# Optimization experiments

Measured on AMD Instinct MI355X. Metric: run time of the kernel, lower is better.

Reference implementation:

```python
import jax, jax.numpy as jnp
import numpy as np

N = 50000      # num nodes
E0 = 400000    # raw directed edges
F = 64         # latent_dim (in and per-head out)
H = 2          # num_heads
L = 2          # num_layers
NEG_SLOPE = 0.2


def _build_edges(src_raw, dst_raw):
    # dgl.to_bidirected(dgl.graph((src,dst))) then add_self_loop
    s = np.asarray(src_raw, dtype=np.int64)
    d = np.asarray(dst_raw, dtype=np.int64)
    s2 = np.concatenate([s, d])
    d2 = np.concatenate([d, s])
    code = np.unique(s2 * N + d2)                      # dedupe (bidirected simple graph)
    s2, d2 = code // N, code % N
    keep = s2 != d2                                    # drop existing self loops
    s2, d2 = s2[keep], d2[keep]
    loops = np.arange(N, dtype=np.int64)
    s2 = np.concatenate([s2, loops])
    d2 = np.concatenate([d2, loops])
    return jnp.asarray(s2, jnp.int32), jnp.asarray(d2, jnp.int32)


def setup_inputs() -> dict:
    key = jax.random.key(0)
    kh, ks, kd, kw1, kb1, kw2, kb2, ka = jax.random.split(key, 8)
    src_raw = jax.random.randint(ks, (E0,), 0, N, dtype=jnp.int32)
    dst_raw = jax.random.randint(kd, (E0,), 0, N, dtype=jnp.int32)
    src, dst = _build_edges(np.asarray(src_raw), np.asarray(dst_raw))
    h = jax.random.normal(kh, (N, F), dtype=jnp.float32)
    scale = 1.0 / np.sqrt(F)
    Wsrc = jax.random.normal(kw1, (L, F, H * F), dtype=jnp.float32) * scale
    bsrc = jnp.zeros((L, H * F), dtype=jnp.float32)
    Wdst = jax.random.normal(kw2, (L, F, H * F), dtype=jnp.float32) * scale
    bdst = jnp.zeros((L, H * F), dtype=jnp.float32)
    attn = jax.random.normal(ka, (L, H, F), dtype=jnp.float32) * scale
    return {"h": h, "Wsrc": Wsrc, "bsrc": bsrc, "Wdst": Wdst, "bdst": bdst,
            "attn": attn, "src": src, "dst": dst}


def _gatv2_layer(h, Wsrc, bsrc, Wdst, bdst, attn, src, dst):
    # h: [N,F] -> per-head projections [N,H,F]
    fs = (h @ Wsrc + bsrc).reshape(N, H, F)
    fd = (h @ Wdst + bdst).reshape(N, H, F)
    # per-edge GATv2 logits: a^T leaky_relu(W_s h_u + W_d h_v)
    e = jax.nn.leaky_relu(fs[src] + fd[dst], NEG_SLOPE)      # [E,H,F]
    logits = jnp.einsum("ehf,hf->eh", e, attn)               # [E,H]
    # edge-softmax over incoming edges of each dst node
    m = jax.ops.segment_max(logits, dst, num_segments=N)     # [N,H]
    ex = jnp.exp(logits - m[dst])
    denom = jax.ops.segment_sum(ex, dst, num_segments=N)     # [N,H]
    alpha = ex / denom[dst]                                  # [E,H]
    # scatter-weighted aggregation
    out = jax.ops.segment_sum(alpha[:, :, None] * fs[src], dst, num_segments=N)  # [N,H,F]
    return out.mean(axis=1)                                  # head mean -> [N,F]


def reference(h, Wsrc, bsrc, Wdst, bdst, attn, src, dst):
    for l in range(L):
        h = _gatv2_layer(h, Wsrc[l], bsrc[l], Wdst[l], bdst[l], attn[l], src, dst)
    return h
```

## Files before the change

kernel.cpp:

```cpp
#include <hip/hip_runtime.h>


#define RLN2 1.4426950408889634f

typedef _Float16 half4v __attribute__((ext_vector_type(4)));

template <int CTRL>
__device__ __forceinline__ float dpp_add(float x) {
  return x + __int_as_float(__builtin_amdgcn_update_dpp(
                 0, __float_as_int(x), CTRL, 0xF, 0xF, true));
}

__device__ __forceinline__ float xor16_add(float x) {
  return x + __int_as_float(
                 __builtin_amdgcn_ds_swizzle(__float_as_int(x), 0x401F));
}

__global__ void rowstart_kernel(const int* __restrict__ src,
                                int* __restrict__ row_start, int EM, int n) {
  int v = blockIdx.x * blockDim.x + threadIdx.x;
  if (v > n) return;
  if (v == n) { row_start[n] = EM; return; }
  int lo = 0, hi = EM;
  while (lo < hi) {
    int mid = (lo + hi) >> 1;
    if (src[mid] < v) lo = mid + 1; else hi = mid;
  }
  row_start[v] = lo;
}

__global__ __launch_bounds__(512) void proj2_kernel(
    const float* __restrict__ hin, const float* __restrict__ Ws,
    const float* __restrict__ bs, const float* __restrict__ Wd,
    const float* __restrict__ bd, _Float16* __restrict__ fs16,
    float* __restrict__ fd, int n) {
  __shared__ float lds[12544];
  int tid = threadIdx.x;
  int tile = blockIdx.x >> 1;
  int half = blockIdx.x & 1;
  int fb = half * 32;
  int row0 = tile * 64;

  const float4* Ws4 = (const float4*)Ws;
  const float4* Wd4 = (const float4*)Wd;
#pragma unroll
  for (int t = 0; t < 2; ++t) {
    int g = tid + t * 512;
    int k = g >> 4, part = (g >> 3) & 1, c4 = g & 7;
    int srcf4 = k * 32 + part * 16 + half * 8 + c4;
    float4 vs = Ws4[srcf4];
    float4 vd = Wd4[srcf4];
    int base = k * 64 + 8 * c4 + part;
    lds[base + 0] = vs.x; lds[base + 2] = vs.y;
    lds[base + 4] = vs.z; lds[base + 6] = vs.w;
    lds[4096 + base + 0] = vd.x; lds[4096 + base + 2] = vd.y;
    lds[4096 + base + 4] = vd.z; lds[4096 + base + 6] = vd.w;
  }
  const float4* h4 = (const float4*)hin;
#pragma unroll
  for (int t = 0; t < 2; ++t) {
    int idx = tid + t * 512;
    int r = idx >> 4, c = idx & 15;
    int rr = min(row0 + r, n - 1);
    *(float4*)&lds[8192 + r * 68 + c * 4] = h4[(size_t)rr * 16 + c];
  }
  __syncthreads();

  const float* WsL = lds;
  const float* WdL = lds + 4096;
  const float* hL = lds + 8192;

  int jh = tid & 15;
  int rg = tid >> 4;
  int r0 = rg * 2;

  float4 as0 = make_float4(0, 0, 0, 0), as1 = make_float4(0, 0, 0, 0);
  float4 ad0 = make_float4(0, 0, 0, 0), ad1 = make_float4(0, 0, 0, 0);

#pragma unroll 4
  for (int k4 = 0; k4 < 16; ++k4) {
    float4 hv0 = *(const float4*)&hL[r0 * 68 + k4 * 4];
    float4 hv1 = *(const float4*)&hL[(r0 + 1) * 68 + k4 * 4];
    float h0a[4] = {hv0.x, hv0.y, hv0.z, hv0.w};
    float h1a[4] = {hv1.x, hv1.y, hv1.z, hv1.w};
#pragma unroll
    for (int kk = 0; kk < 4; ++kk) {
      int k = k4 * 4 + kk;
      float4 ws = *(const float4*)&WsL[k * 64 + jh * 4];
      float4 wd = *(const float4*)&WdL[k * 64 + jh * 4];
      as0.x = fmaf(h0a[kk], ws.x, as0.x); as0.y = fmaf(h0a[kk], ws.y, as0.y);
      as0.z = fmaf(h0a[kk], ws.z, as0.z); as0.w = fmaf(h0a[kk], ws.w, as0.w);
      as1.x = fmaf(h1a[kk], ws.x, as1.x); as1.y = fmaf(h1a[kk], ws.y, as1.y);
      as1.z = fmaf(h1a[kk], ws.z, as1.z); as1.w = fmaf(h1a[kk], ws.w, as1.w);
      ad0.x = fmaf(h0a[kk], wd.x, ad0.x); ad0.y = fmaf(h0a[kk], wd.y, ad0.y);
      ad0.z = fmaf(h0a[kk], wd.z, ad0.z); ad0.w = fmaf(h0a[kk], wd.w, ad0.w);
      ad1.x = fmaf(h1a[kk], wd.x, ad1.x); ad1.y = fmaf(h1a[kk], wd.y, ad1.y);
      ad1.z = fmaf(h1a[kk], wd.z, ad1.z); ad1.w = fmaf(h1a[kk], wd.w, ad1.w);
    }
  }

  int j0 = fb + 2 * jh, j1 = j0 + 1;
  float4 bsv = make_float4(bs[j0], bs[64 + j0], bs[j1], bs[64 + j1]);
  float4 bdv = make_float4(bd[j0], bd[64 + j0], bd[j1], bd[64 + j1]);
  int col = half * 16 + jh;
  float4* fd4 = (float4*)fd;
  half4v* fsH = (half4v*)fs16;
#pragma unroll
  for (int r = 0; r < 2; ++r) {
    int rr = row0 + r0 + r;
    if (rr < n) {
      float4 a = r ? as1 : as0;
      float4 d = r ? ad1 : ad0;
      fd4[(size_t)rr * 32 + col] = make_float4(d.x + bdv.x, d.y + bdv.y,
                                               d.z + bdv.z, d.w + bdv.w);
      half4v hv;
      hv.x = (_Float16)(a.x + bsv.x); hv.y = (_Float16)(a.y + bsv.y);
      hv.z = (_Float16)(a.z + bsv.z); hv.w = (_Float16)(a.w + bsv.w);
      fsH[(size_t)rr * 32 + col] = hv;
    }
  }
}

__global__ __launch_bounds__(256) void gat_node_kernel(
    const _Float16* __restrict__ fs16, const float* __restrict__ fd,
    const float* __restrict__ attn, const int* __restrict__ row_start,
    const int* __restrict__ nbr, float* __restrict__ out, int n) {
  int wid = (int)((blockIdx.x * 256 + threadIdx.x) >> 6);
  int lane = threadIdx.x & 63;
  if (wid >= n) return;
  int lp = lane & 15;
  int slot = lane >> 4;

  float aAx = attn[2 * lp] * RLN2;
  float aAy = attn[64 + 2 * lp] * RLN2;
  float aAz = attn[2 * lp + 1] * RLN2;
  float aAw = attn[64 + 2 * lp + 1] * RLN2;
  float aBx = attn[32 + 2 * lp] * RLN2;
  float aBy = attn[96 + 2 * lp] * RLN2;
  float aBz = attn[32 + 2 * lp + 1] * RLN2;
  float aBw = attn[96 + 2 * lp + 1] * RLN2;

  const half4v* fsH = (const half4v*)fs16;
  const float4* fd4 = (const float4*)fd;
  float4 fdA = fd4[(size_t)wid * 32 + lp];
  float4 fdB = fd4[(size_t)wid * 32 + 16 + lp];

  float4 accA = make_float4(0, 0, 0, 0), accB = make_float4(0, 0, 0, 0);
  float d0 = 0.f, d1 = 0.f;

  {
    half4v sa = fsH[(size_t)wid * 32 + lp];
    half4v sb = fsH[(size_t)wid * 32 + 16 + lp];
    float4 xA = make_float4((float)sa.x, (float)sa.y, (float)sa.z, (float)sa.w);
    float4 xB = make_float4((float)sb.x, (float)sb.y, (float)sb.z, (float)sb.w);
    float t, m, p0, p1;
    t = xA.x + fdA.x; m = fmaxf(t, 0.2f * t); p0 = aAx * m;
    t = xA.y + fdA.y; m = fmaxf(t, 0.2f * t); p1 = aAy * m;
    t = xA.z + fdA.z; m = fmaxf(t, 0.2f * t); p0 = fmaf(aAz, m, p0);
    t = xA.w + fdA.w; m = fmaxf(t, 0.2f * t); p1 = fmaf(aAw, m, p1);
    t = xB.x + fdB.x; m = fmaxf(t, 0.2f * t); p0 = fmaf(aBx, m, p0);
    t = xB.y + fdB.y; m = fmaxf(t, 0.2f * t); p1 = fmaf(aBy, m, p1);
    t = xB.z + fdB.z; m = fmaxf(t, 0.2f * t); p0 = fmaf(aBz, m, p0);
    t = xB.w + fdB.w; m = fmaxf(t, 0.2f * t); p1 = fmaf(aBw, m, p1);
    p0 = dpp_add<0xB1>(p0);  p1 = dpp_add<0xB1>(p1);
    p0 = dpp_add<0x4E>(p0);  p1 = dpp_add<0x4E>(p1);
    p0 = dpp_add<0x141>(p0); p1 = dpp_add<0x141>(p1);
    p0 = dpp_add<0x140>(p0); p1 = dpp_add<0x140>(p1);
    float w0 = __builtin_amdgcn_exp2f(p0);
    float w1 = __builtin_amdgcn_exp2f(p1);
    if (slot != 0) { w0 = 0.f; w1 = 0.f; }
    d0 += w0; d1 += w1;
    accA.x = fmaf(w0, xA.x, accA.x); accA.y = fmaf(w1, xA.y, accA.y);
    accA.z = fmaf(w0, xA.z, accA.z); accA.w = fmaf(w1, xA.w, accA.w);
    accB.x = fmaf(w0, xB.x, accB.x); accB.y = fmaf(w1, xB.y, accB.y);
    accB.z = fmaf(w0, xB.z, accB.z); accB.w = fmaf(w1, xB.w, accB.w);
  }

  int e0 = row_start[wid], e1 = row_start[wid + 1];
  if (e0 < e1) {
    int last = e1 - 1;
    int u0 = nbr[min(e0 + slot, last)];
    half4v a0 = fsH[(size_t)u0 * 32 + lp];
    half4v b0 = fsH[(size_t)u0 * 32 + 16 + lp];
    int uN = nbr[min(e0 + 4 + slot, last)];

    for (int i = e0; i < e1; i += 4) {
      int uNN = nbr[min(i + 8 + slot, last)];
      half4v a1 = fsH[(size_t)uN * 32 + lp];
      half4v b1 = fsH[(size_t)uN * 32 + 16 + lp];

      float4 xA = make_float4((float)a0.x, (float)a0.y, (float)a0.z, (float)a0.w);
      float4 xB = make_float4((float)b0.x, (float)b0.y, (float)b0.z, (float)b0.w);
      float t, m, p0, p1;
      t = xA.x + fdA.x; m = fmaxf(t, 0.2f * t); p0 = aAx * m;
      t = xA.y + fdA.y; m = fmaxf(t, 0.2f * t); p1 = aAy * m;
      t = xA.z + fdA.z; m = fmaxf(t, 0.2f * t); p0 = fmaf(aAz, m, p0);
      t = xA.w + fdA.w; m = fmaxf(t, 0.2f * t); p1 = fmaf(aAw, m, p1);
      t = xB.x + fdB.x; m = fmaxf(t, 0.2f * t); p0 = fmaf(aBx, m, p0);
      t = xB.y + fdB.y; m = fmaxf(t, 0.2f * t); p1 = fmaf(aBy, m, p1);
      t = xB.z + fdB.z; m = fmaxf(t, 0.2f * t); p0 = fmaf(aBz, m, p0);
      t = xB.w + fdB.w; m = fmaxf(t, 0.2f * t); p1 = fmaf(aBw, m, p1);
      p0 = dpp_add<0xB1>(p0);  p1 = dpp_add<0xB1>(p1);
      p0 = dpp_add<0x4E>(p0);  p1 = dpp_add<0x4E>(p1);
      p0 = dpp_add<0x141>(p0); p1 = dpp_add<0x141>(p1);
      p0 = dpp_add<0x140>(p0); p1 = dpp_add<0x140>(p1);
      float w0 = __builtin_amdgcn_exp2f(p0);
      float w1 = __builtin_amdgcn_exp2f(p1);
      if (i + slot >= e1) { w0 = 0.f; w1 = 0.f; }
      d0 += w0; d1 += w1;
      accA.x = fmaf(w0, xA.x, accA.x); accA.y = fmaf(w1, xA.y, accA.y);
      accA.z = fmaf(w0, xA.z, accA.z); accA.w = fmaf(w1, xA.w, accA.w);
      accB.x = fmaf(w0, xB.x, accB.x); accB.y = fmaf(w1, xB.y, accB.y);
      accB.z = fmaf(w0, xB.z, accB.z); accB.w = fmaf(w1, xB.w, accB.w);

      a0 = a1; b0 = b1; uN = uNN;
    }
  }

  accA.x = xor16_add(accA.x); accA.y = xor16_add(accA.y);
  accA.z = xor16_add(accA.z); accA.w = xor16_add(accA.w);
  accB.x = xor16_add(accB.x); accB.y = xor16_add(accB.y);
  accB.z = xor16_add(accB.z); accB.w = xor16_add(accB.w);
  d0 = xor16_add(d0); d1 = xor16_add(d1);
  accA.x += __shfl_xor(accA.x, 32, 64); accA.y += __shfl_xor(accA.y, 32, 64);
  accA.z += __shfl_xor(accA.z, 32, 64); accA.w += __shfl_xor(accA.w, 32, 64);
  accB.x += __shfl_xor(accB.x, 32, 64); accB.y += __shfl_xor(accB.y, 32, 64);
  accB.z += __shfl_xor(accB.z, 32, 64); accB.w += __shfl_xor(accB.w, 32, 64);
  d0 += __shfl_xor(d0, 32, 64); d1 += __shfl_xor(d1, 32, 64);

  if (lane < 16) {
    float rd0 = 1.0f / d0, rd1 = 1.0f / d1;
    float2 oA = make_float2(0.5f * (accA.x * rd0 + accA.y * rd1),
                            0.5f * (accA.z * rd0 + accA.w * rd1));
    float2 oB = make_float2(0.5f * (accB.x * rd0 + accB.y * rd1),
                            0.5f * (accB.z * rd0 + accB.w * rd1));
    float2* o2 = (float2*)out;
    o2[(size_t)wid * 32 + lp] = oA;
    o2[(size_t)wid * 32 + 16 + lp] = oB;
  }
}

extern "C" void kernel_launch(void* const* d_in, const int* in_sizes, int n_in,
                              void* d_out, int out_size, void* d_ws, size_t ws_size,
                              hipStream_t stream) {
  const float* h    = (const float*)d_in[0];
  const float* Wsrc = (const float*)d_in[1];
  const float* bsrc = (const float*)d_in[2];
  const float* Wdst = (const float*)d_in[3];
  const float* bdst = (const float*)d_in[4];
  const float* attn = (const float*)d_in[5];
  const int*   src  = (const int*)d_in[6];
  const int*   dst  = (const int*)d_in[7];
  int E = in_sizes[6];
  int N = in_sizes[0] / 64;
  int EM = E - N;
  float* out = (float*)d_out;

  float*     fd        = (float*)d_ws;
  _Float16*  fs16      = (_Float16*)(fd + (size_t)N * 128);
  int*       row_start = (int*)(fs16 + (size_t)N * 128);

  rowstart_kernel<<<(N + 256) / 256, 256, 0, stream>>>(src, row_start, EM, N);

  int pb = ((N + 63) / 64) * 2;
  int nb = (N + 3) / 4;
  for (int l = 0; l < 2; ++l) {
    const float* hin = (l == 0) ? h : out;
    proj2_kernel<<<pb, 512, 0, stream>>>(hin, Wsrc + (size_t)l * 64 * 128,
                                         bsrc + (size_t)l * 128,
                                         Wdst + (size_t)l * 64 * 128,
                                         bdst + (size_t)l * 128, fs16, fd, N);
    gat_node_kernel<<<nb, 256, 0, stream>>>(fs16, fd, attn + (size_t)l * 128,
                                            row_start, dst, out, N);
  }
}
```

Baseline: 164.2 us.

## Compute edge logits in packed fp16 with dot2 and store fd as fp16 head-major

The destination projection is now stored in fp16 rather than fp32, and both projections switch to a head-major layout. The per-edge leaky-ReLU and attention dot product are computed with packed half4 math and fdot2 instead of scalar fp32 FMAs. The aim is to cut the fd write/read bytes and the VALU instruction count in the hot edge loop, and the output store becomes a single float4 per lane. The trade-off is lower precision in the logits, since the sum, leaky-ReLU and attention weights are all fp16, which may hurt accuracy.

```diff
diff --git a/kernel.cpp b/kernel.cpp
--- a/kernel.cpp
+++ b/kernel.cpp
@@ -4,6 +4,7 @@
 #define RLN2 1.4426950408889634f
 
 typedef _Float16 half4v __attribute__((ext_vector_type(4)));
+typedef _Float16 half2v __attribute__((ext_vector_type(2)));
 
 template <int CTRL>
 __device__ __forceinline__ float dpp_add(float x) {
@@ -14,6 +15,21 @@
 __device__ __forceinline__ float xor16_add(float x) {
   return x + __int_as_float(
                  __builtin_amdgcn_ds_swizzle(__float_as_int(x), 0x401F));
+}
+
+__device__ __forceinline__ float dot2(half2v a, half2v b, float c) {
+#if __has_builtin(__builtin_amdgcn_fdot2)
+  return __builtin_amdgcn_fdot2(a, b, c, false);
+#else
+  return fmaf((float)a.x, (float)b.x, fmaf((float)a.y, (float)b.y, c));
+#endif
+}
+
+__device__ __forceinline__ half2v lo2(half4v v) {
+  return __builtin_shufflevector(v, v, 0, 1);
+}
+__device__ __forceinline__ half2v hi2(half4v v) {
+  return __builtin_shufflevector(v, v, 2, 3);
 }
 
 __global__ void rowstart_kernel(const int* __restrict__ src,
@@ -33,7 +49,7 @@
     const float* __restrict__ hin, const float* __restrict__ Ws,
     const float* __restrict__ bs, const float* __restrict__ Wd,
     const float* __restrict__ bd, _Float16* __restrict__ fs16,
-    float* __restrict__ fd, int n) {
+    _Float16* __restrict__ fd16, int n) {
   __shared__ float lds[12544];
   int tid = threadIdx.x;
   int tile = blockIdx.x >> 1;
@@ -102,27 +118,53 @@
   int j0 = fb + 2 * jh, j1 = j0 + 1;
   float4 bsv = make_float4(bs[j0], bs[64 + j0], bs[j1], bs[64 + j1]);
   float4 bdv = make_float4(bd[j0], bd[64 + j0], bd[j1], bd[64 + j1]);
-  int col = half * 16 + jh;
-  float4* fd4 = (float4*)fd;
-  half4v* fsH = (half4v*)fs16;
 #pragma unroll
   for (int r = 0; r < 2; ++r) {
     int rr = row0 + r0 + r;
     if (rr < n) {
       float4 a = r ? as1 : as0;
       float4 d = r ? ad1 : ad0;
-      fd4[(size_t)rr * 32 + col] = make_float4(d.x + bdv.x, d.y + bdv.y,
-                                               d.z + bdv.z, d.w + bdv.w);
-      half4v hv;
-      hv.x = (_Float16)(a.x + bsv.x); hv.y = (_Float16)(a.y + bsv.y);
-      hv.z = (_Float16)(a.z + bsv.z); hv.w = (_Float16)(a.w + bsv.w);
-      fsH[(size_t)rr * 32 + col] = hv;
+      half2v s_h0 = {(_Float16)(a.x + bsv.x), (_Float16)(a.z + bsv.z)};
+      half2v s_h1 = {(_Float16)(a.y + bsv.y), (_Float16)(a.w + bsv.w)};
+      half2v d_h0 = {(_Float16)(d.x + bdv.x), (_Float16)(d.z + bdv.z)};
+      half2v d_h1 = {(_Float16)(d.y + bdv.y), (_Float16)(d.w + bdv.w)};
+      *(half2v*)&fs16[(size_t)rr * 128 + j0] = s_h0;
+      *(half2v*)&fs16[(size_t)rr * 128 + 64 + j0] = s_h1;
+      *(half2v*)&fd16[(size_t)rr * 128 + j0] = d_h0;
+      *(half2v*)&fd16[(size_t)rr * 128 + 64 + j0] = d_h1;
     }
   }
 }
 
+#define EDGE_LOGIT(x0, x1, p0, p1)                                      \
+  {                                                                     \
+    half4v t0 = (x0) + fdh0;                                            \
+    half4v t1 = (x1) + fdh1;                                            \
+    half4v m0 = __builtin_elementwise_max(t0, t0 * c02);                \
+    half4v m1 = __builtin_elementwise_max(t1, t1 * c02);                \
+    p0 = dot2(hi2(m0), a0hi, dot2(lo2(m0), a0lo, 0.f));                 \
+    p1 = dot2(hi2(m1), a1hi, dot2(lo2(m1), a1lo, 0.f));                 \
+    p0 = dpp_add<0xB1>(p0);  p1 = dpp_add<0xB1>(p1);                    \
+    p0 = dpp_add<0x4E>(p0);  p1 = dpp_add<0x4E>(p1);                    \
+    p0 = dpp_add<0x141>(p0); p1 = dpp_add<0x141>(p1);                   \
+    p0 = dpp_add<0x140>(p0); p1 = dpp_add<0x140>(p1);                   \
+  }
+
+#define EDGE_ACC(x0, x1, w0, w1)                                        \
+  {                                                                     \
+    d0 += (w0); d1 += (w1);                                             \
+    acc0.x = fmaf((w0), (float)(x0).x, acc0.x);                         \
+    acc0.y = fmaf((w0), (float)(x0).y, acc0.y);                         \
+    acc0.z = fmaf((w0), (float)(x0).z, acc0.z);                         \
+    acc0.w = fmaf((w0), (float)(x0).w, acc0.w);                         \
+    acc1.x = fmaf((w1), (float)(x1).x, acc1.x);                         \
+    acc1.y = fmaf((w1), (float)(x1).y, acc1.y);                         \
+    acc1.z = fmaf((w1), (float)(x1).z, acc1.z);                         \
+    acc1.w = fmaf((w1), (float)(x1).w, acc1.w);                         \
+  }
+
 __global__ __launch_bounds__(256) void gat_node_kernel(
-    const _Float16* __restrict__ fs16, const float* __restrict__ fd,
+    const _Float16* __restrict__ fs16, const _Float16* __restrict__ fd16,
     const float* __restrict__ attn, const int* __restrict__ row_start,
     const int* __restrict__ nbr, float* __restrict__ out, int n) {
   int wid = (int)((blockIdx.x * 256 + threadIdx.x) >> 6);
@@ -131,112 +173,79 @@
   int lp = lane & 15;
   int slot = lane >> 4;
 
-  float aAx = attn[2 * lp] * RLN2;
-  float aAy = attn[64 + 2 * lp] * RLN2;
-  float aAz = attn[2 * lp + 1] * RLN2;
-  float aAw = attn[64 + 2 * lp + 1] * RLN2;
-  float aBx = attn[32 + 2 * lp] * RLN2;
-  float aBy = attn[96 + 2 * lp] * RLN2;
-  float aBz = attn[32 + 2 * lp + 1] * RLN2;
-  float aBw = attn[96 + 2 * lp + 1] * RLN2;
+  half2v a0lo = {(_Float16)(attn[4 * lp] * RLN2),
+                 (_Float16)(attn[4 * lp + 1] * RLN2)};
+  half2v a0hi = {(_Float16)(attn[4 * lp + 2] * RLN2),
+                 (_Float16)(attn[4 * lp + 3] * RLN2)};
+  half2v a1lo = {(_Float16)(attn[64 + 4 * lp] * RLN2),
+                 (_Float16)(attn[64 + 4 * lp + 1] * RLN2)};
+  half2v a1hi = {(_Float16)(attn[64 + 4 * lp + 2] * RLN2),
+                 (_Float16)(attn[64 + 4 * lp + 3] * RLN2)};
+  const half4v c02 = {(_Float16)0.2f, (_Float16)0.2f, (_Float16)0.2f,
+                      (_Float16)0.2f};
 
   const half4v* fsH = (const half4v*)fs16;
-  const float4* fd4 = (const float4*)fd;
-  float4 fdA = fd4[(size_t)wid * 32 + lp];
-  float4 fdB = fd4[(size_t)wid * 32 + 16 + lp];
-
-  float4 accA = make_float4(0, 0, 0, 0), accB = make_float4(0, 0, 0, 0);
+  const half4v* fdH = (const half4v*)fd16;
+  half4v fdh0 = fdH[(size_t)wid * 32 + lp];
+  half4v fdh1 = fdH[(size_t)wid * 32 + 16 + lp];
+
+  float4 acc0 = make_float4(0, 0, 0, 0), acc1 = make_float4(0, 0, 0, 0);
   float d0 = 0.f, d1 = 0.f;
 
   {
-    half4v sa = fsH[(size_t)wid * 32 + lp];
-    half4v sb = fsH[(size_t)wid * 32 + 16 + lp];
-    float4 xA = make_float4((float)sa.x, (float)sa.y, (float)sa.z, (float)sa.w);
-    float4 xB = make_float4((float)sb.x, (float)sb.y, (float)sb.z, (float)sb.w);
-    float t, m, p0, p1;
-    t = xA.x + fdA.x; m = fmaxf(t, 0.2f * t); p0 = aAx * m;
-    t = xA.y + fdA.y; m = fmaxf(t, 0.2f * t); p1 = aAy * m;
-    t = xA.z + fdA.z; m = fmaxf(t, 0.2f * t); p0 = fmaf(aAz, m, p0);
-    t = xA.w + fdA.w; m = fmaxf(t, 0.2f * t); p1 = fmaf(aAw, m, p1);
-    t = xB.x + fdB.x; m = fmaxf(t, 0.2f * t); p0 = fmaf(aBx, m, p0);
-    t = xB.y + fdB.y; m = fmaxf(t, 0.2f * t); p1 = fmaf(aBy, m, p1);
-    t = xB.z + fdB.z; m = fmaxf(t, 0.2f * t); p0 = fmaf(aBz, m, p0);
-    t = xB.w + fdB.w; m = fmaxf(t, 0.2f * t); p1 = fmaf(aBw, m, p1);
-    p0 = dpp_add<0xB1>(p0);  p1 = dpp_add<0xB1>(p1);
-    p0 = dpp_add<0x4E>(p0);  p1 = dpp_add<0x4E>(p1);
-    p0 = dpp_add<0x141>(p0); p1 = dpp_add<0x141>(p1);
-    p0 = dpp_add<0x140>(p0); p1 = dpp_add<0x140>(p1);
+    half4v x0 = fsH[(size_t)wid * 32 + lp];
+    half4v x1 = fsH[(size_t)wid * 32 + 16 + lp];
+    float p0, p1;
+    EDGE_LOGIT(x0, x1, p0, p1);
     float w0 = __builtin_amdgcn_exp2f(p0);
     float w1 = __builtin_amdgcn_exp2f(p1);
     if (slot != 0) { w0 = 0.f; w1 = 0.f; }
-    d0 += w0; d1 += w1;
-    accA.x = fmaf(w0, xA.x, accA.x); accA.y = fmaf(w1, xA.y, accA.y);
-    accA.z = fmaf(w0, xA.z, accA.z); accA.w = fmaf(w1, xA.w, accA.w);
-    accB.x = fmaf(w0, xB.x, accB.x); accB.y = fmaf(w1, xB.y, accB.y);
-    accB.z = fmaf(w0, xB.z, accB.z); accB.w = fmaf(w1, xB.w, accB.w);
+    EDGE_ACC(x0, x1, w0, w1);
   }
 
   int e0 = row_start[wid], e1 = row_start[wid + 1];
   if (e0 < e1) {
     int last = e1 - 1;
     int u0 = nbr[min(e0 + slot, last)];
-    half4v a0 = fsH[(size_t)u0 * 32 + lp];
-    half4v b0 = fsH[(size_t)u0 * 32 + 16 + lp];
+    half4v xa = fsH[(size_t)u0 * 32 + lp];
+    half4v xb = fsH[(size_t)u0 * 32 + 16 + lp];
     int uN = nbr[min(e0 + 4 + slot, last)];
 
     for (int i = e0; i < e1; i += 4) {
       int uNN = nbr[min(i + 8 + slot, last)];
-      half4v a1 = fsH[(size_t)uN * 32 + lp];
-      half4v b1 = fsH[(size_t)uN * 32 + 16 + lp];
-
-      float4 xA = make_float4((float)a0.x, (float)a0.y, (float)a0.z, (float)a0.w);
-      float4 xB = make_float4((float)b0.x, (float)b0.y, (float)b0.z, (float)b0.w);
-      float t, m, p0, p1;
-      t = xA.x + fdA.x; m = fmaxf(t, 0.2f * t); p0 = aAx * m;
-      t = xA.y + fdA.y; m = fmaxf(t, 0.2f * t); p1 = aAy * m;
-      t = xA.z + fdA.z; m = fmaxf(t, 0.2f * t); p0 = fmaf(aAz, m, p0);
-      t = xA.w + fdA.w; m = fmaxf(t, 0.2f * t); p1 = fmaf(aAw, m, p1);
-      t = xB.x + fdB.x; m = fmaxf(t, 0.2f * t); p0 = fmaf(aBx, m, p0);
-      t = xB.y + fdB.y; m = fmaxf(t, 0.2f * t); p1 = fmaf(aBy, m, p1);
-      t = xB.z + fdB.z; m = fmaxf(t, 0.2f * t); p0 = fmaf(aBz, m, p0);
-      t = xB.w + fdB.w; m = fmaxf(t, 0.2f * t); p1 = fmaf(aBw, m, p1);
-      p0 = dpp_add<0xB1>(p0);  p1 = dpp_add<0xB1>(p1);
-      p0 = dpp_add<0x4E>(p0);  p1 = dpp_add<0x4E>(p1);
-      p0 = dpp_add<0x141>(p0); p1 = dpp_add<0x141>(p1);
-      p0 = dpp_add<0x140>(p0); p1 = dpp_add<0x140>(p1);
+      half4v na = fsH[(size_t)uN * 32 + lp];
+      half4v nb = fsH[(size_t)uN * 32 + 16 + lp];
+
+      float p0, p1;
+      EDGE_LOGIT(xa, xb, p0, p1);
       float w0 = __builtin_amdgcn_exp2f(p0);
       float w1 = __builtin_amdgcn_exp2f(p1);
       if (i + slot >= e1) { w0 = 0.f; w1 = 0.f; }
-      d0 += w0; d1 += w1;
-      accA.x = fmaf(w0, xA.x, accA.x); accA.y = fmaf(w1, xA.y, accA.y);
-      accA.z = fmaf(w0, xA.z, accA.z); accA.w = fmaf(w1, xA.w, accA.w);
-      accB.x = fmaf(w0, xB.x, accB.x); accB.y = fmaf(w1, xB.y, accB.y);
-      accB.z = fmaf(w0, xB.z, accB.z); accB.w = fmaf(w1, xB.w, accB.w);
-
-      a0 = a1; b0 = b1; uN = uNN;
+      EDGE_ACC(xa, xb, w0, w1);
+
+      xa = na; xb = nb; uN = uNN;
     }
   }
 
-  accA.x = xor16_add(accA.x); accA.y = xor16_add(accA.y);
-  accA.z = xor16_add(accA.z); accA.w = xor16_add(accA.w);
-  accB.x = xor16_add(accB.x); accB.y = xor16_add(accB.y);
-  accB.z = xor16_add(accB.z); accB.w = xor16_add(accB.w);
+  acc0.x = xor16_add(acc0.x); acc0.y = xor16_add(acc0.y);
+  acc0.z = xor16_add(acc0.z); acc0.w = xor16_add(acc0.w);
+  acc1.x = xor16_add(acc1.x); acc1.y = xor16_add(acc1.y);
+  acc1.z = xor16_add(acc1.z); acc1.w = xor16_add(acc1.w);
   d0 = xor16_add(d0); d1 = xor16_add(d1);
-  accA.x += __shfl_xor(accA.x, 32, 64); accA.y += __shfl_xor(accA.y, 32, 64);
-  accA.z += __shfl_xor(accA.z, 32, 64); accA.w += __shfl_xor(accA.w, 32, 64);
-  accB.x += __shfl_xor(accB.x, 32, 64); accB.y += __shfl_xor(accB.y, 32, 64);
-  accB.z += __shfl_xor(accB.z, 32, 64); accB.w += __shfl_xor(accB.w, 32, 64);
+  acc0.x += __shfl_xor(acc0.x, 32, 64); acc0.y += __shfl_xor(acc0.y, 32, 64);
+  acc0.z += __shfl_xor(acc0.z, 32, 64); acc0.w += __shfl_xor(acc0.w, 32, 64);
+  acc1.x += __shfl_xor(acc1.x, 32, 64); acc1.y += __shfl_xor(acc1.y, 32, 64);
+  acc1.z += __shfl_xor(acc1.z, 32, 64); acc1.w += __shfl_xor(acc1.w, 32, 64);
   d0 += __shfl_xor(d0, 32, 64); d1 += __shfl_xor(d1, 32, 64);
 
   if (lane < 16) {
     float rd0 = 1.0f / d0, rd1 = 1.0f / d1;
-    float2 oA = make_float2(0.5f * (accA.x * rd0 + accA.y * rd1),
-                            0.5f * (accA.z * rd0 + accA.w * rd1));
-    float2 oB = make_float2(0.5f * (accB.x * rd0 + accB.y * rd1),
-                            0.5f * (accB.z * rd0 + accB.w * rd1));
-    float2* o2 = (float2*)out;
-    o2[(size_t)wid * 32 + lp] = oA;
-    o2[(size_t)wid * 32 + 16 + lp] = oB;
+    float4 o;
+    o.x = 0.5f * (acc0.x * rd0 + acc1.x * rd1);
+    o.y = 0.5f * (acc0.y * rd0 + acc1.y * rd1);
+    o.z = 0.5f * (acc0.z * rd0 + acc1.z * rd1);
+    o.w = 0.5f * (acc0.w * rd0 + acc1.w * rd1);
+    ((float4*)out)[(size_t)wid * 16 + lp] = o;
   }
 }
 
@@ -256,9 +265,9 @@
   int EM = E - N;
   float* out = (float*)d_out;
 
-  float*     fd        = (float*)d_ws;
-  _Float16*  fs16      = (_Float16*)(fd + (size_t)N * 128);
-  int*       row_start = (int*)(fs16 + (size_t)N * 128);
+  _Float16* fs16      = (_Float16*)d_ws;
+  _Float16* fd16      = fs16 + (size_t)N * 128;
+  int*      row_start = (int*)(fd16 + (size_t)N * 128);
 
   rowstart_kernel<<<(N + 256) / 256, 256, 0, stream>>>(src, row_start, EM, N);
 
@@ -269,8 +278,8 @@
     proj2_kernel<<<pb, 512, 0, stream>>>(hin, Wsrc + (size_t)l * 64 * 128,
                                          bsrc + (size_t)l * 128,
                                          Wdst + (size_t)l * 64 * 128,
-                                         bdst + (size_t)l * 128, fs16, fd, N);
-    gat_node_kernel<<<nb, 256, 0, stream>>>(fs16, fd, attn + (size_t)l * 128,
+                                         bdst + (size_t)l * 128, fs16, fd16, N);
+    gat_node_kernel<<<nb, 256, 0, stream>>>(fs16, fd16, attn + (size_t)l * 128,
                                             row_start, dst, out, N);
   }
 }
```

Result: no change. 161.5 us (-1.6%).
